# Optimization experiments

Measured on AMD Instinct MI355X. Metric: run time of the kernel, lower is better.

Reference implementation:

```python
import jax, jax.numpy as jnp
import numpy as np

B, A, C = 1, 196416, 90
H = W = 1024
SCORE_THRESHOLD = 0.05
MAX_DETECTIONS = 100
# RetinaNet-style BBoxTransform normalization (mean=0, std=[0.1,0.1,0.2,0.2])
STD = (0.1, 0.1, 0.2, 0.2)


def setup_inputs() -> dict:
    key = jax.random.key(0)
    k1, k2, k3, k4, k5, k6, k7 = jax.random.split(key, 7)
    x = jax.random.normal(k1, (B, 3, H, W), dtype=jnp.float32)
    regression = jax.random.normal(k2, (B, A, 4), dtype=jnp.float32) * 0.1
    classification = jax.random.normal(k3, (B, A, C), dtype=jnp.float32)
    # valid anchor boxes (x1, y1, x2, y2)
    cx = jax.random.uniform(k4, (B, A), minval=0.0, maxval=float(W))
    cy = jax.random.uniform(k5, (B, A), minval=0.0, maxval=float(H))
    aw = jax.random.uniform(k6, (B, A), minval=16.0, maxval=256.0)
    ah = jax.random.uniform(k7, (B, A), minval=16.0, maxval=256.0)
    anchors = jnp.stack([cx - 0.5 * aw, cy - 0.5 * ah, cx + 0.5 * aw, cy + 0.5 * ah], axis=2).astype(jnp.float32)
    return {"x": x, "regression": regression, "classification": classification, "anchors": anchors}


def _decode_clip(anchors, regression, img_h, img_w):
    # BBoxTransform: deltas (dx, dy, dw, dh) scaled by std, applied to anchor center/size
    wa = anchors[..., 2] - anchors[..., 0]
    ha = anchors[..., 3] - anchors[..., 1]
    cxa = anchors[..., 0] + 0.5 * wa
    cya = anchors[..., 1] + 0.5 * ha
    dx = regression[..., 0] * STD[0]
    dy = regression[..., 1] * STD[1]
    dw = regression[..., 2] * STD[2]
    dh = regression[..., 3] * STD[3]
    cx = cxa + dx * wa
    cy = cya + dy * ha
    w = jnp.exp(dw) * wa
    h = jnp.exp(dh) * ha
    # ClipBoxes: x1,y1 clamped at 0; x2,y2 clamped at image width/height
    x1 = jnp.maximum(cx - 0.5 * w, 0.0)
    y1 = jnp.maximum(cy - 0.5 * h, 0.0)
    x2 = jnp.minimum(cx + 0.5 * w, float(img_w))
    y2 = jnp.minimum(cy + 0.5 * h, float(img_h))
    return jnp.stack([x1, y1, x2, y2], axis=2)  # [B, A, 4]


def reference(x, regression, classification, anchors):
    img_h, img_w = x.shape[2], x.shape[3]
    boxes = _decode_clip(anchors, regression, img_h, img_w)  # [1, A, 4]
    probs = jax.nn.sigmoid(classification)                    # [1, A, C]
    scores = jnp.max(probs, axis=2)                           # [1, A]
    classes = jnp.argmax(probs, axis=2)                       # [1, A]
    valid_scores = jnp.where(scores > SCORE_THRESHOLD, scores, 0.0)
    vb = boxes[0]            # [A, 4]
    vc = classes[0]          # [A]
    vs = valid_scores[0]     # [A]
    k = min(MAX_DETECTIONS, vs.shape[0])
    _, top_idx = jax.lax.top_k(vs, k)
    final_boxes = vb[top_idx]
    final_scores = vs[top_idx]
    final_classes = vc[top_idx]
    return (final_boxes, final_scores, final_classes)
```

## Files before the change

kernel.cpp:

```cpp
#include <hip/hip_runtime.h>
#include <cmath>

#define A_CNT 196416
#define C_CNT 90
#define QUADS (A_CNT / 4)
#define QITERS (QUADS / 8)
#define TOPK 100u
#define CAPB 2048
#define NB_RED 512
#define NWAVES 2048
#define NB_GAT 192

#define OFF_HIST1 785664u
#define OFF_CTRL  789760u
#define OFF_CANDA 789824u
#define OFF_CANDB 790336u

#define AGENT_LD(p)    __hip_atomic_load((p), __ATOMIC_RELAXED, __HIP_MEMORY_SCOPE_AGENT)
#define AGENT_ST(p, v) __hip_atomic_store((p), (v), __ATOMIC_RELAXED, __HIP_MEMORY_SCOPE_AGENT)


#define LOADQ(V, qq)                                                        \
    {                                                                       \
        const float4* __restrict__ r4_ = cls4 + (size_t)(qq) * 90;          \
        _Pragma("unroll")                                                   \
        for (int i_ = 0; i_ < 12; ++i_) {                                   \
            const int j_ = s + 8 * i_;                                      \
            V[i_] = r4_[(j_ < 90) ? j_ : 89];   \
        }                                                                   \
    }                                                                       \
    __builtin_amdgcn_sched_barrier(0);

#define REDUCE_EMIT(V, qq)                                                  \
    {                                                                       \
        float m0 = -INFINITY, m1 = -INFINITY, m2 = -INFINITY, m3 = -INFINITY; \
        _Pragma("unroll")                                                   \
        for (int i_ = 0; i_ < 12; ++i_) {                                   \
            const int j_ = s + 8 * i_;                                      \
            const float4 vv = V[i_];                                        \
            const float a01 = fmaxf(vv.x, vv.y), a23 = fmaxf(vv.z, vv.w);   \
            const float all = fmaxf(a01, a23);                              \
            if (j_ < 22)       m0 = fmaxf(m0, all);                         \
            else if (j_ == 22) { m0 = fmaxf(m0, a01); m1 = fmaxf(m1, a23); }\
            else if (j_ < 45)  m1 = fmaxf(m1, all);                         \
            else if (j_ < 67)  m2 = fmaxf(m2, all);                         \
            else if (j_ == 67) { m2 = fmaxf(m2, a01); m3 = fmaxf(m3, a23); }\
            else if (j_ < 90)  m3 = fmaxf(m3, all);                         \
        }                                                                   \
        _Pragma("unroll")                                                   \
        for (int d_ = 1; d_ < 8; d_ <<= 1) {                                \
            m0 = fmaxf(m0, __shfl_xor(m0, d_));                             \
            m1 = fmaxf(m1, __shfl_xor(m1, d_));                             \
            m2 = fmaxf(m2, __shfl_xor(m2, d_));                             \
            m3 = fmaxf(m3, __shfl_xor(m3, d_));                             \
        }                                                                   \
        if (s == 0) {                                                       \
            float p0 = 1.0f / (1.0f + expf(-m0));    \
            float p1 = 1.0f / (1.0f + expf(-m1));                           \
            float p2 = 1.0f / (1.0f + expf(-m2));                           \
            float p3 = 1.0f / (1.0f + expf(-m3));                           \
            unsigned k0 = (p0 > 0.05f) ? __float_as_uint(p0) : 0u;          \
            unsigned k1 = (p1 > 0.05f) ? __float_as_uint(p1) : 0u;          \
            unsigned k2 = (p2 > 0.05f) ? __float_as_uint(p2) : 0u;          \
            unsigned k3 = (p3 > 0.05f) ? __float_as_uint(p3) : 0u;          \
            *(uint4*)(keys + 4 * (size_t)(qq)) = make_uint4(k0, k1, k2, k3);\
            unsigned h0 = k0 ? (min(k0 >> 16, 0x3F80u) - 0x3D4Bu) : 0u;     \
            unsigned h1 = k1 ? (min(k1 >> 16, 0x3F80u) - 0x3D4Bu) : 0u;     \
            unsigned h2 = k2 ? (min(k2 >> 16, 0x3F80u) - 0x3D4Bu) : 0u;     \
            unsigned h3 = k3 ? (min(k3 >> 16, 0x3F80u) - 0x3D4Bu) : 0u;     \
            atomicAdd(&lhist[h0], 1u);                                      \
            atomicAdd(&lhist[h1], 1u);                                      \
            atomicAdd(&lhist[h2], 1u);                                      \
            atomicAdd(&lhist[h3], 1u);                                      \
        }                                                                   \
    }

__global__ __launch_bounds__(256, 2) void k_reduce(const float* __restrict__ cls,
                                                   unsigned* __restrict__ keys,
                                                   unsigned* __restrict__ hist1,
                                                   unsigned* __restrict__ ctrl) {
    __shared__ unsigned lhist[576];
    __shared__ unsigned sdata[256];
    __shared__ unsigned sbin[2];
    __shared__ int sflag;
    const int t = threadIdx.x;
    for (int j = t; j < 576; j += 256) lhist[j] = 0u;
    __syncthreads();

    const int lane = t & 63;
    const int g = lane >> 3, s = lane & 7;
    const int w = blockIdx.x * 4 + (t >> 6);
    const float4* __restrict__ cls4 = (const float4*)cls;

    const int qi0 = w;
    const int qi1 = w + NWAVES;
    const int qi2 = w + 2 * NWAVES;
    const bool has2 = (qi2 < QITERS);
    const int q0 = qi0 * 8 + g;
    const int q1 = qi1 * 8 + g;
    const int q2 = (has2 ? qi2 : qi0) * 8 + g;

    float4 vA[12], vB[12];
    LOADQ(vA, q0);
    LOADQ(vB, q1);
    REDUCE_EMIT(vA, q0);
    LOADQ(vA, q2);
    REDUCE_EMIT(vB, q1);
    if (has2) REDUCE_EMIT(vA, q2);

    __syncthreads();
    for (int j = t; j < 576; j += 256) {
        unsigned c = lhist[j];
        if (c) atomicAdd(&hist1[j], c);
    }
    __syncthreads();
    if (t == 0) sflag = (atomicAdd(&ctrl[8], 1u) == NB_RED - 1u) ? 1 : 0;
    __syncthreads();
    if (!sflag) return;

    const unsigned target = TOPK;
    unsigned ssum = 0;
#pragma unroll
    for (int j = 0; j < 4; ++j) ssum += AGENT_LD(&hist1[t * 4 + j]);
    sdata[t] = ssum;
    for (int d = 1; d < 256; d <<= 1) {
        __syncthreads();
        unsigned add = (t + d < 256) ? sdata[t + d] : 0u;
        __syncthreads();
        sdata[t] += add;
    }
    __syncthreads();
    {
        unsigned mysuf  = sdata[t];
        unsigned nxtsuf = (t < 255) ? sdata[t + 1] : 0u;
        if (nxtsuf < target && mysuf >= target) { sbin[0] = (unsigned)t; sbin[1] = nxtsuf; }
    }
    __syncthreads();
    const unsigned chunkB = sbin[0];
    const unsigned gAbove = sbin[1];
    unsigned v = (t < 4) ? AGENT_LD(&hist1[chunkB * 4 + t]) : 0u;
    sdata[t] = v;
    for (int d = 1; d < 256; d <<= 1) {
        __syncthreads();
        unsigned add = (t + d < 256) ? sdata[t + d] : 0u;
        __syncthreads();
        sdata[t] += add;
    }
    __syncthreads();
    {
        unsigned mysuf  = sdata[t] + gAbove;
        unsigned nxtsuf = ((t < 255) ? sdata[t + 1] : 0u) + gAbove;
        if (nxtsuf < target && mysuf >= target) {
            unsigned bin = chunkB * 4 + (unsigned)t;
            ctrl[0] = bin ? (bin + 0x3D4Bu) : 0u;
            ctrl[1] = nxtsuf;
        }
    }
}

__global__ __launch_bounds__(256) void k_gather(const float* __restrict__ cls,
                                                const float* __restrict__ reg,
                                                const float* __restrict__ anc,
                                                const unsigned* __restrict__ keys,
                                                unsigned* __restrict__ ctrl,
                                                unsigned* __restrict__ candA,
                                                unsigned* __restrict__ candB,
                                                float* __restrict__ out) {
    __shared__ unsigned sAi[128], sAk[128];
    __shared__ unsigned sBi[CAPB], sBk[CAPB];
    __shared__ unsigned sel[TOPK];
    __shared__ int sflag;
    const int t = threadIdx.x;

    const unsigned binB = ctrl[0];
    const int i4 = blockIdx.x * 256 + t;
    if (i4 < A_CNT / 4) {
        uint4 k = ((const uint4*)keys)[i4];
        const unsigned base = (unsigned)(4 * i4);
#pragma unroll
        for (int j = 0; j < 4; ++j) {
            unsigned kk = (j == 0) ? k.x : (j == 1) ? k.y : (j == 2) ? k.z : k.w;
            unsigned t16 = kk >> 16;
            if (t16 > binB) {
                unsigned q = atomicAdd(&ctrl[5], 1u);
                if (q < 128u) AGENT_ST(&candA[q], base + j);
            } else if (t16 == binB) {
                unsigned q = atomicAdd(&ctrl[6], 1u);
                if (q < (unsigned)CAPB) AGENT_ST(&candB[q], base + j);
            }
        }
    }
    __syncthreads();
    if (t == 0) sflag = (atomicAdd(&ctrl[9], 1u) == (unsigned)NB_GAT - 1u) ? 1 : 0;
    __syncthreads();
    if (!sflag) return;

    const unsigned nA = min(AGENT_LD(&ctrl[5]), 128u);
    const unsigned nB = min(AGENT_LD(&ctrl[6]), (unsigned)CAPB);
    const unsigned need = TOPK - nA;

    if (t < (int)nA) { unsigned i = AGENT_LD(&candA[t]); sAi[t] = i; sAk[t] = keys[i]; }
    for (unsigned e = (unsigned)t; e < nB; e += 256u) {
        unsigned i = AGENT_LD(&candB[e]); sBi[e] = i; sBk[e] = keys[i];
    }
    __syncthreads();

    if (t < (int)nA) {
        unsigned mi = sAi[t], mk = sAk[t], r = 0;
        for (unsigned j = 0; j < nA; ++j) {
            unsigned ok = sAk[j];
            if (ok > mk || (ok == mk && sAi[j] < mi)) r++;
        }
        sel[r] = mi;
    }
    for (unsigned e = (unsigned)t; e < nB; e += 256u) {
        unsigned mi = sBi[e], mk = sBk[e], r = 0;
        for (unsigned j = 0; j < nB; ++j) {
            unsigned ok = sBk[j];
            if (ok > mk || (ok == mk && sBi[j] < mi)) r++;
        }
        if (r < need) sel[nA + r] = mi;
    }
    __syncthreads();

    if (t < (int)TOPK) {
        const unsigned a = sel[t];
        const float2* __restrict__ row = (const float2*)(cls + (size_t)a * C_CNT);
        float2 vr[45];
#pragma unroll
        for (int c = 0; c < 45; ++c) vr[c] = row[c];
        float bv = -INFINITY; int bi = 0;
#pragma unroll
        for (int c = 0; c < 45; ++c) {
            if (vr[c].x > bv) { bv = vr[c].x; bi = 2 * c; }
            if (vr[c].y > bv) { bv = vr[c].y; bi = 2 * c + 1; }
        }
        float score = __uint_as_float(keys[a]);
        const float4 an = ((const float4*)anc)[a];
        const float4 rg = ((const float4*)reg)[a];
        float wa = an.z - an.x, ha = an.w - an.y;
        float cxa = an.x + 0.5f * wa, cya = an.y + 0.5f * ha;
        float dx = rg.x * 0.1f, dy = rg.y * 0.1f;
        float dw = rg.z * 0.2f, dh = rg.w * 0.2f;
        float cx = cxa + dx * wa, cy = cya + dy * ha;
        float w = expf(dw) * wa, h = expf(dh) * ha;
        out[t * 4 + 0] = fmaxf(cx - 0.5f * w, 0.0f);
        out[t * 4 + 1] = fmaxf(cy - 0.5f * h, 0.0f);
        out[t * 4 + 2] = fminf(cx + 0.5f * w, 1024.0f);
        out[t * 4 + 3] = fminf(cy + 0.5f * h, 1024.0f);
        out[400 + t] = score;
        out[500 + t] = (float)bi;
    }
}

extern "C" void kernel_launch(void* const* d_in, const int* in_sizes, int n_in,
                              void* d_out, int out_size, void* d_ws, size_t ws_size,
                              hipStream_t stream) {
    const float* reg = (const float*)d_in[1];
    const float* cls = (const float*)d_in[2];
    const float* anc = (const float*)d_in[3];
    float* out = (float*)d_out;
    char* ws = (char*)d_ws;
    unsigned* keys  = (unsigned*)ws;
    unsigned* hist1 = (unsigned*)(ws + OFF_HIST1);
    unsigned* ctrl  = (unsigned*)(ws + OFF_CTRL);
    unsigned* candA = (unsigned*)(ws + OFF_CANDA);
    unsigned* candB = (unsigned*)(ws + OFF_CANDB);

    hipMemsetAsync(hist1, 0, 4096 + 64, stream);
    k_reduce<<<NB_RED, 256, 0, stream>>>(cls, keys, hist1, ctrl);
    k_gather<<<NB_GAT, 256, 0, stream>>>(cls, reg, anc, keys, ctrl, candA, candB, out);
}
```

Before: 133.9 us.

## Add second-level radix histogram to prune tie-bin ranking; preload third reduce tile

In the gather tail, candidates from the boundary bin are histogrammed on key bits 8-15 and suffix-scanned to find a sub-bin threshold. Only candidates at or above that sub-bin are ranked, each against its own group, which replaces the full O(nB^2) rank over the boundary bin. The reduce kernel now issues all three tile loads up front into a third register array, trading extra VGPRs for more memory-level parallelism. Selected scores are kept in shared memory instead of being reloaded from the keys buffer.

```diff
diff --git a/kernel.cpp b/kernel.cpp
--- a/kernel.cpp
+++ b/kernel.cpp
@@ -75,6 +75,15 @@
         }                                                                   \
     }
 
+#define SUFFIX_SCAN_SDATA()                                                 \
+    for (int d_ = 1; d_ < 256; d_ <<= 1) {                                  \
+        __syncthreads();                                                    \
+        unsigned add_ = (t + d_ < 256) ? sdata[t + d_] : 0u;                \
+        __syncthreads();                                                    \
+        sdata[t] += add_;                                                   \
+    }                                                                       \
+    __syncthreads();
+
 __global__ __launch_bounds__(256, 2) void k_reduce(const float* __restrict__ cls,
                                                    unsigned* __restrict__ keys,
                                                    unsigned* __restrict__ hist1,
@@ -92,21 +101,19 @@
     const int w = blockIdx.x * 4 + (t >> 6);
     const float4* __restrict__ cls4 = (const float4*)cls;
 
-    const int qi0 = w;
-    const int qi1 = w + NWAVES;
     const int qi2 = w + 2 * NWAVES;
     const bool has2 = (qi2 < QITERS);
-    const int q0 = qi0 * 8 + g;
-    const int q1 = qi1 * 8 + g;
-    const int q2 = (has2 ? qi2 : qi0) * 8 + g;
-
-    float4 vA[12], vB[12];
+    const int q0 = w * 8 + g;
+    const int q1 = (w + NWAVES) * 8 + g;
+    const int q2 = (has2 ? qi2 : w) * 8 + g;
+
+    float4 vA[12], vB[12], vC[12];
     LOADQ(vA, q0);
     LOADQ(vB, q1);
+    LOADQ(vC, q2);
     REDUCE_EMIT(vA, q0);
-    LOADQ(vA, q2);
     REDUCE_EMIT(vB, q1);
-    if (has2) REDUCE_EMIT(vA, q2);
+    if (has2) REDUCE_EMIT(vC, q2);
 
     __syncthreads();
     for (int j = t; j < 576; j += 256) {
@@ -118,39 +125,25 @@
     __syncthreads();
     if (!sflag) return;
 
-    const unsigned target = TOPK;
     unsigned ssum = 0;
 #pragma unroll
     for (int j = 0; j < 4; ++j) ssum += AGENT_LD(&hist1[t * 4 + j]);
     sdata[t] = ssum;
-    for (int d = 1; d < 256; d <<= 1) {
-        __syncthreads();
-        unsigned add = (t + d < 256) ? sdata[t + d] : 0u;
-        __syncthreads();
-        sdata[t] += add;
-    }
-    __syncthreads();
+    SUFFIX_SCAN_SDATA()
     {
         unsigned mysuf  = sdata[t];
         unsigned nxtsuf = (t < 255) ? sdata[t + 1] : 0u;
-        if (nxtsuf < target && mysuf >= target) { sbin[0] = (unsigned)t; sbin[1] = nxtsuf; }
+        if (nxtsuf < TOPK && mysuf >= TOPK) { sbin[0] = (unsigned)t; sbin[1] = nxtsuf; }
     }
     __syncthreads();
     const unsigned chunkB = sbin[0];
     const unsigned gAbove = sbin[1];
-    unsigned v = (t < 4) ? AGENT_LD(&hist1[chunkB * 4 + t]) : 0u;
-    sdata[t] = v;
-    for (int d = 1; d < 256; d <<= 1) {
-        __syncthreads();
-        unsigned add = (t + d < 256) ? sdata[t + d] : 0u;
-        __syncthreads();
-        sdata[t] += add;
-    }
-    __syncthreads();
+    sdata[t] = (t < 4) ? AGENT_LD(&hist1[chunkB * 4 + t]) : 0u;
+    SUFFIX_SCAN_SDATA()
     {
         unsigned mysuf  = sdata[t] + gAbove;
         unsigned nxtsuf = ((t < 255) ? sdata[t + 1] : 0u) + gAbove;
-        if (nxtsuf < target && mysuf >= target) {
+        if (nxtsuf < TOPK && mysuf >= TOPK) {
             unsigned bin = chunkB * 4 + (unsigned)t;
             ctrl[0] = bin ? (bin + 0x3D4Bu) : 0u;
             ctrl[1] = nxtsuf;
@@ -168,7 +161,9 @@
                                                 float* __restrict__ out) {
     __shared__ unsigned sAi[128], sAk[128];
     __shared__ unsigned sBi[CAPB], sBk[CAPB];
-    __shared__ unsigned sel[TOPK];
+    __shared__ unsigned sdata[256];
+    __shared__ unsigned sbin[2];
+    __shared__ unsigned sel[TOPK], selk[TOPK];
     __shared__ int sflag;
     const int t = threadIdx.x;
 
@@ -203,7 +198,19 @@
     for (unsigned e = (unsigned)t; e < nB; e += 256u) {
         unsigned i = AGENT_LD(&candB[e]); sBi[e] = i; sBk[e] = keys[i];
     }
-    __syncthreads();
+    sdata[t] = 0u;
+    __syncthreads();
+    for (unsigned e = (unsigned)t; e < nB; e += 256u)
+        atomicAdd(&sdata[(sBk[e] >> 8) & 0xFFu], 1u);
+    SUFFIX_SCAN_SDATA()
+    {
+        unsigned mysuf  = sdata[t];
+        unsigned nxtsuf = (t < 255) ? sdata[t + 1] : 0u;
+        if (nxtsuf < need && mysuf >= need) { sbin[0] = (unsigned)t; sbin[1] = nxtsuf; }
+    }
+    __syncthreads();
+    const unsigned bstar = sbin[0];
+    const unsigned S1    = sbin[1];
 
     if (t < (int)nA) {
         unsigned mi = sAi[t], mk = sAk[t], r = 0;
@@ -211,15 +218,28 @@
             unsigned ok = sAk[j];
             if (ok > mk || (ok == mk && sAi[j] < mi)) r++;
         }
-        sel[r] = mi;
+        sel[r] = mi; selk[r] = mk;
     }
     for (unsigned e = (unsigned)t; e < nB; e += 256u) {
-        unsigned mi = sBi[e], mk = sBk[e], r = 0;
-        for (unsigned j = 0; j < nB; ++j) {
-            unsigned ok = sBk[j];
-            if (ok > mk || (ok == mk && sBi[j] < mi)) r++;
-        }
-        if (r < need) sel[nA + r] = mi;
+        unsigned mk = sBk[e], mi = sBi[e];
+        unsigned mb = (mk >> 8) & 0xFFu;
+        if (mb > bstar) {
+            unsigned r = 0;
+            for (unsigned j = 0; j < nB; ++j) {
+                unsigned ok = sBk[j];
+                if (((ok >> 8) & 0xFFu) > bstar &&
+                    (ok > mk || (ok == mk && sBi[j] < mi))) r++;
+            }
+            sel[nA + r] = mi; selk[nA + r] = mk;
+        } else if (mb == bstar) {
+            unsigned r = 0;
+            for (unsigned j = 0; j < nB; ++j) {
+                unsigned ok = sBk[j];
+                if (((ok >> 8) & 0xFFu) == bstar &&
+                    (ok > mk || (ok == mk && sBi[j] < mi))) r++;
+            }
+            if (r < need - S1) { sel[nA + S1 + r] = mi; selk[nA + S1 + r] = mk; }
+        }
     }
     __syncthreads();
 
@@ -235,7 +255,7 @@
             if (vr[c].x > bv) { bv = vr[c].x; bi = 2 * c; }
             if (vr[c].y > bv) { bv = vr[c].y; bi = 2 * c + 1; }
         }
-        float score = __uint_as_float(keys[a]);
+        float score = __uint_as_float(selk[t]);
         const float4 an = ((const float4*)anc)[a];
         const float4 rg = ((const float4*)reg)[a];
         float wa = an.z - an.x, ha = an.w - an.y;
@@ -243,11 +263,11 @@
         float dx = rg.x * 0.1f, dy = rg.y * 0.1f;
         float dw = rg.z * 0.2f, dh = rg.w * 0.2f;
         float cx = cxa + dx * wa, cy = cya + dy * ha;
-        float w = expf(dw) * wa, h = expf(dh) * ha;
-        out[t * 4 + 0] = fmaxf(cx - 0.5f * w, 0.0f);
-        out[t * 4 + 1] = fmaxf(cy - 0.5f * h, 0.0f);
-        out[t * 4 + 2] = fminf(cx + 0.5f * w, 1024.0f);
-        out[t * 4 + 3] = fminf(cy + 0.5f * h, 1024.0f);
+        float w2 = expf(dw) * wa, h2 = expf(dh) * ha;
+        out[t * 4 + 0] = fmaxf(cx - 0.5f * w2, 0.0f);
+        out[t * 4 + 1] = fmaxf(cy - 0.5f * h2, 0.0f);
+        out[t * 4 + 2] = fminf(cx + 0.5f * w2, 1024.0f);
+        out[t * 4 + 3] = fminf(cy + 0.5f * h2, 1024.0f);
         out[400 + t] = score;
         out[500 + t] = (float)bi;
     }
```

New measurement: 155.6 us. 16.2% more time.
